# Optimization experiments

Measured on AMD Instinct MI355X. Metric: run time of the kernel, lower is better.

Reference implementation:

```python
import jax, jax.numpy as jnp
import numpy as np

N = 20000   # nodes
E = 320000  # edges (before self loops)
H = 4       # heads
HID = 64    # hidden per head
EMB = 32    # embedding dim
IN = 4      # input features
SLOPE = 0.2   # GATv2 leaky_relu negative slope
BN_EPS = 1e-5


def _gatv2(x, Wl, bl, Wr, br, att, bias, src, dst, heads, out_ch, concat, n_nodes):
    # PyG GATv2Conv (share_weights=False, add_self_loops handled by caller)
    xl = (x @ Wl.T + bl).reshape(n_nodes, heads, out_ch)  # source transform (x_j)
    xr = (x @ Wr.T + br).reshape(n_nodes, heads, out_ch)  # target transform (x_i)
    e = jax.nn.leaky_relu(xl[src] + xr[dst], SLOPE)       # [E, H, C]
    score = jnp.einsum('ehc,hc->eh', e, att)              # [E, H]
    smax = jax.ops.segment_max(score, dst, num_segments=n_nodes)
    expw = jnp.exp(score - smax[dst])
    denom = jax.ops.segment_sum(expw, dst, num_segments=n_nodes)
    alpha = expw / (denom[dst] + 1e-16)                   # segment softmax over dst
    out = jax.ops.segment_sum(xl[src] * alpha[:, :, None], dst, num_segments=n_nodes)
    out = out.reshape(n_nodes, heads * out_ch) if concat else out.mean(axis=1)
    return out + bias


def _bn(x, gamma, beta, mean, var):
    # BatchNorm1d, eval mode (running stats)
    return gamma * (x - mean) * jax.lax.rsqrt(var + BN_EPS) + beta


def setup_inputs() -> dict:
    key = jax.random.key(0)
    ks = iter(jax.random.split(key, 40))
    d = {}
    d['x'] = jax.random.normal(next(ks), (N, IN), dtype=jnp.float32)
    d['edge_index'] = jax.random.randint(next(ks), (2, E), 0, N, dtype=jnp.int32)

    def lin(k, o, i):
        return (jax.random.normal(k, (o, i), dtype=jnp.float32) * (1.0 / np.sqrt(i)))

    d['Wl1'] = lin(next(ks), H * HID, IN); d['bl1'] = jnp.zeros((H * HID,), jnp.float32)
    d['Wr1'] = lin(next(ks), H * HID, IN); d['br1'] = jnp.zeros((H * HID,), jnp.float32)
    d['att1'] = jax.random.normal(next(ks), (H, HID), dtype=jnp.float32) * 0.1
    d['bias1'] = jnp.zeros((H * HID,), jnp.float32)
    d['bn1_g'] = jnp.ones((H * HID,), jnp.float32)
    d['bn1_b'] = jnp.zeros((H * HID,), jnp.float32)
    d['bn1_m'] = jax.random.normal(next(ks), (H * HID,), dtype=jnp.float32) * 0.1
    d['bn1_v'] = jax.random.uniform(next(ks), (H * HID,), dtype=jnp.float32) + 0.5

    d['Wl2'] = lin(next(ks), H * HID, H * HID); d['bl2'] = jnp.zeros((H * HID,), jnp.float32)
    d['Wr2'] = lin(next(ks), H * HID, H * HID); d['br2'] = jnp.zeros((H * HID,), jnp.float32)
    d['att2'] = jax.random.normal(next(ks), (H, HID), dtype=jnp.float32) * 0.1
    d['bias2'] = jnp.zeros((H * HID,), jnp.float32)
    d['bn2_g'] = jnp.ones((H * HID,), jnp.float32)
    d['bn2_b'] = jnp.zeros((H * HID,), jnp.float32)
    d['bn2_m'] = jax.random.normal(next(ks), (H * HID,), dtype=jnp.float32) * 0.1
    d['bn2_v'] = jax.random.uniform(next(ks), (H * HID,), dtype=jnp.float32) + 0.5

    # layer 3: 256 -> 32, 1 head, mean (concat=False)
    d['Wl3'] = lin(next(ks), EMB, H * HID); d['bl3'] = jnp.zeros((EMB,), jnp.float32)
    d['Wr3'] = lin(next(ks), EMB, H * HID); d['br3'] = jnp.zeros((EMB,), jnp.float32)
    d['att3'] = jax.random.normal(next(ks), (1, EMB), dtype=jnp.float32) * 0.1
    d['bias3'] = jnp.zeros((EMB,), jnp.float32)
    return d


def reference(x, edge_index,
              Wl1, bl1, Wr1, br1, att1, bias1, bn1_g, bn1_b, bn1_m, bn1_v,
              Wl2, bl2, Wr2, br2, att2, bias2, bn2_g, bn2_b, bn2_m, bn2_v,
              Wl3, bl3, Wr3, br3, att3, bias3):
    # add self loops (PyG default add_self_loops=True)
    loops = jnp.arange(N, dtype=edge_index.dtype)
    src = jnp.concatenate([edge_index[0], loops])
    dst = jnp.concatenate([edge_index[1], loops])

    h = _gatv2(x, Wl1, bl1, Wr1, br1, att1, bias1, src, dst, H, HID, True, N)
    h = jax.nn.elu(_bn(h, bn1_g, bn1_b, bn1_m, bn1_v))  # dropout: eval mode -> identity
    h = _gatv2(h, Wl2, bl2, Wr2, br2, att2, bias2, src, dst, H, HID, True, N)
    h = jax.nn.elu(_bn(h, bn2_g, bn2_b, bn2_m, bn2_v))
    z = _gatv2(h, Wl3, bl3, Wr3, br3, att3, bias3, src, dst, 1, EMB, False, N)
    return z
```

## Files before the change

### kernel.cpp

```cpp
#include <hip/hip_runtime.h>
#include <math.h>

#define NN 20000
#define EE 320000
#define ETOT (EE + NN)
#define NSCAN ((NN + 1023) / 1024)

typedef unsigned short ushort_t;
typedef unsigned int uint_t;
typedef __attribute__((ext_vector_type(8))) short bf16x8;
typedef __attribute__((ext_vector_type(4))) float f32x4;

__device__ __forceinline__ ushort_t f2bf(float f) {
  union { float f; uint_t u; } v; v.f = f;
  uint_t r = v.u + 0x7FFF + ((v.u >> 16) & 1);
  return (ushort_t)(r >> 16);
}
__device__ __forceinline__ float bf2f(uint_t hi16) {
  union { uint_t u; float f; } v; v.u = hi16 << 16;
  return v.f;
}
__device__ __forceinline__ uint_t pack2(float a, float b) {
  return (uint_t)f2bf(a) | ((uint_t)f2bf(b) << 16);
}
__device__ __forceinline__ void unpack8(uint4 u, float* x) {
  x[0] = bf2f(u.x & 0xFFFF); x[1] = bf2f(u.x >> 16);
  x[2] = bf2f(u.y & 0xFFFF); x[3] = bf2f(u.y >> 16);
  x[4] = bf2f(u.z & 0xFFFF); x[5] = bf2f(u.z >> 16);
  x[6] = bf2f(u.w & 0xFFFF); x[7] = bf2f(u.w >> 16);
}

__global__ void deg_kernel(const int* __restrict__ ei, int* __restrict__ deg) {
  int e = blockIdx.x * 256 + threadIdx.x;
  if (e >= ETOT) return;
  int dst = (e < EE) ? ei[EE + e] : (e - EE);
  atomicAdd(&deg[dst], 1);
}

__global__ __launch_bounds__(1024) void scan1_kernel(const int* __restrict__ deg,
                                                     int* __restrict__ rowptr,
                                                     int* __restrict__ partials) {
  __shared__ int wsum[16];
  const int tid = threadIdx.x;
  const int lane = tid & 63, wid = tid >> 6;
  int i = blockIdx.x * 1024 + tid;
  int v = (i < NN) ? deg[i] : 0;
  int x = v;
  #pragma unroll
  for (int off = 1; off < 64; off <<= 1) {
    int y = __shfl_up(x, off, 64);
    if (lane >= off) x += y;
  }
  if (lane == 63) wsum[wid] = x;
  __syncthreads();
  if (tid < 64) {
    int w = (tid < 16) ? wsum[tid] : 0;
    #pragma unroll
    for (int off = 1; off < 16; off <<= 1) {
      int y = __shfl_up(w, off, 64);
      if (lane >= off) w += y;
    }
    if (tid < 16) wsum[tid] = w;
  }
  __syncthreads();
  int incl = x + (wid > 0 ? wsum[wid - 1] : 0);
  if (i < NN) rowptr[i] = incl - v;
  if (tid == 1023) partials[blockIdx.x] = incl;
}

__global__ void scan2_kernel(int* __restrict__ partials, int* __restrict__ rowptr) {
  int lane = threadIdx.x;
  int v = (lane < NSCAN) ? partials[lane] : 0;
  int x = v;
  #pragma unroll
  for (int off = 1; off < 64; off <<= 1) {
    int y = __shfl_up(x, off, 64);
    if (lane >= off) x += y;
  }
  if (lane < NSCAN) partials[lane] = x - v;
  if (lane == 63) rowptr[NN] = x;
}

__global__ __launch_bounds__(1024) void scan3_kernel(int* __restrict__ rowptr,
                                                     const int* __restrict__ partials,
                                                     int* __restrict__ cursor) {
  int i = blockIdx.x * 1024 + threadIdx.x;
  if (i < NN) {
    int r = rowptr[i] + partials[blockIdx.x];
    rowptr[i] = r;
    cursor[i] = r;
  }
}

__global__ void fill_kernel(const int* __restrict__ ei, int* __restrict__ cursor,
                            int* __restrict__ csr_src) {
  int e = blockIdx.x * 256 + threadIdx.x;
  if (e >= ETOT) return;
  int src, dst;
  if (e < EE) { src = ei[e]; dst = ei[EE + e]; } else { src = dst = e - EE; }
  int slot = atomicAdd(&cursor[dst], 1);
  csr_src[slot] = src;
}

__global__ void lin1_w2bf(const float* __restrict__ x,
                          const float* __restrict__ Wl, const float* __restrict__ bl,
                          const float* __restrict__ Wr, const float* __restrict__ br,
                          ushort_t* __restrict__ xlr,
                          const float* __restrict__ W0, const float* __restrict__ W1,
                          const float* __restrict__ W2, const float* __restrict__ W3,
                          ushort_t* __restrict__ Wb) {
  if (blockIdx.x >= NN) {
    int i = (blockIdx.x - NN) * 256 + threadIdx.x;
    if (i < 65536) Wb[i] = f2bf(W0[i]);
    else if (i < 131072) Wb[i] = f2bf(W1[i - 65536]);
    else if (i < 139264) Wb[i] = f2bf(W2[i - 131072]);
    else if (i < 147456) Wb[i] = f2bf(W3[i - 139264]);
    return;
  }
  int n = blockIdx.x, o = threadIdx.x;
  float4 xv = *reinterpret_cast<const float4*>(x + (size_t)n * 4);
  float4 wl = *reinterpret_cast<const float4*>(Wl + (size_t)o * 4);
  float4 wr = *reinterpret_cast<const float4*>(Wr + (size_t)o * 4);
  xlr[(size_t)n * 512 + o]       = f2bf(wl.x * xv.x + wl.y * xv.y + wl.z * xv.z + wl.w * xv.w + bl[o]);
  xlr[(size_t)n * 512 + 256 + o] = f2bf(wr.x * xv.x + wr.y * xv.y + wr.z * xv.z + wr.w * xv.w + br[o]);
}

template<int N, int NL, int WMW, int WNW>
__global__ __launch_bounds__(WMW * WNW * 64) void gemm_mfma(
    const ushort_t* __restrict__ X, const ushort_t* __restrict__ Wb,
    const float* __restrict__ bl, const float* __restrict__ br,
    ushort_t* __restrict__ Y, int M) {
  const int wave = threadIdx.x >> 6;
  const int lane = threadIdx.x & 63;
  const int wm = wave / WNW, wn = wave % WNW;
  const int r16 = lane & 15;
  const int koff = (lane >> 4) * 8;
  const int m0 = blockIdx.x * (WMW * 64) + wm * 64;
  const int nb = blockIdx.y * (WNW * 64) + wn * 64;

  const ushort_t* xp = X + (size_t)(m0 + r16) * 256 + koff;
  const ushort_t* wp = Wb + (size_t)(nb + r16) * 256 + koff;

  f32x4 acc[4][4] = {};
  bf16x8 A[4], B[4], An[4], Bn[4];
  #pragma unroll
  for (int i = 0; i < 4; ++i) {
    A[i] = *reinterpret_cast<const bf16x8*>(xp + i * 16 * 256);
    B[i] = *reinterpret_cast<const bf16x8*>(wp + i * 16 * 256);
  }
  #pragma unroll
  for (int t = 0; t < 8; ++t) {
    if (t < 7) {
      const int k0 = (t + 1) * 32;
      #pragma unroll
      for (int i = 0; i < 4; ++i) {
        An[i] = *reinterpret_cast<const bf16x8*>(xp + i * 16 * 256 + k0);
        Bn[i] = *reinterpret_cast<const bf16x8*>(wp + i * 16 * 256 + k0);
      }
    }
    #pragma unroll
    for (int j = 0; j < 4; ++j)
      #pragma unroll
      for (int i = 0; i < 4; ++i)
        acc[j][i] = __builtin_amdgcn_mfma_f32_16x16x32_bf16(B[j], A[i], acc[j][i], 0, 0, 0);
    #pragma unroll
    for (int i = 0; i < 4; ++i) { A[i] = An[i]; B[i] = Bn[i]; }
  }

  const int nlocal = (lane >> 4) * 2;
  #pragma unroll
  for (int j = 0; j < 4; ++j) {
    const int ncol0 = nb + j * 16 + (lane >> 4) * 4;
    const float4 bv = *reinterpret_cast<const float4*>(
        (ncol0 < NL) ? (bl + ncol0) : (br + (ncol0 - NL)));
    #pragma unroll
    for (int i = 0; i < 4; ++i) {
      int m = m0 + i * 16 + r16;
      if (m < M) {
        uint2 o;
        o.x = pack2(acc[j][i][0] + bv.x, acc[j][i][1] + bv.y);
        o.y = pack2(acc[j][i][2] + bv.z, acc[j][i][3] + bv.w);
        *reinterpret_cast<uint2*>(Y + (size_t)m * N + ncol0) = o;
      }
    }
  }
}

template<bool BN_ELU>
__global__ __launch_bounds__(256) void fused_agg4(
    const ushort_t* __restrict__ xlr,
    const int* __restrict__ rowptr, const int* __restrict__ csr_src,
    const float* __restrict__ att, const float* __restrict__ bias,
    const float* __restrict__ bn_g, const float* __restrict__ bn_b,
    const float* __restrict__ bn_m, const float* __restrict__ bn_v,
    ushort_t* __restrict__ out) {
  int n = blockIdx.x * 4 + (threadIdx.x >> 6);
  if (n >= NN) return;
  int lane = threadIdx.x & 63;
  int half = lane >> 5;
  int l32 = lane & 31;

  float xr[8], at[8];
  {
    uint4 xru = reinterpret_cast<const uint4*>(xlr + (size_t)n * 512 + 256)[l32];
    unpack8(xru, xr);
    float4 a0 = reinterpret_cast<const float4*>(att)[l32 * 2];
    float4 a1 = reinterpret_cast<const float4*>(att)[l32 * 2 + 1];
    at[0] = a0.x; at[1] = a0.y; at[2] = a0.z; at[3] = a0.w;
    at[4] = a1.x; at[5] = a1.y; at[6] = a1.z; at[7] = a1.w;
  }
  int beg = rowptr[n], end = rowptr[n + 1];

  float m = -3.4e38f, d = 0.f;
  float acc[8] = {0.f, 0.f, 0.f, 0.f, 0.f, 0.f, 0.f, 0.f};

  for (int s = beg + half; s < end; s += 2) {
    int src = csr_src[s];
    uint4 xu = reinterpret_cast<const uint4*>(xlr + (size_t)src * 512)[l32];
    float x[8];
    unpack8(xu, x);
    float sc = 0.f;
    #pragma unroll
    for (int c = 0; c < 8; ++c) {
      float e = x[c] + xr[c];
      e = fmaxf(e, 0.2f * e);
      sc = fmaf(at[c], e, sc);
    }
    #pragma unroll
    for (int off = 4; off; off >>= 1) sc += __shfl_xor(sc, off, 64);
    if (__any(sc > m + 8.f)) {
      float mn = fmaxf(m, sc);
      float scl = __expf(m - mn);
      float w = __expf(sc - mn);
      #pragma unroll
      for (int c = 0; c < 8; ++c) acc[c] = fmaf(w, x[c], acc[c] * scl);
      d = d * scl + w;
      m = mn;
    } else {
      float w = __expf(sc - m);
      #pragma unroll
      for (int c = 0; c < 8; ++c) acc[c] = fmaf(w, x[c], acc[c]);
      d += w;
    }
  }

  {
    float mo = __shfl_xor(m, 32, 64);
    float doo = __shfl_xor(d, 32, 64);
    float ao[8];
    #pragma unroll
    for (int c = 0; c < 8; ++c) ao[c] = __shfl_xor(acc[c], 32, 64);
    if (doo > 0.f) {
      if (d > 0.f) {
        float mn = fmaxf(m, mo);
        float se = __expf(m - mn), so = __expf(mo - mn);
        #pragma unroll
        for (int c = 0; c < 8; ++c) acc[c] = acc[c] * se + ao[c] * so;
        d = d * se + doo * so;
      } else {
        #pragma unroll
        for (int c = 0; c < 8; ++c) acc[c] = ao[c];
        d = doo;
      }
    }
  }

  if (half == 0) {
    float inv = 1.f / (d + 1e-16f);
    float4 b0 = reinterpret_cast<const float4*>(bias)[l32 * 2];
    float4 b1 = reinterpret_cast<const float4*>(bias)[l32 * 2 + 1];
    float v[8];
    v[0] = acc[0] * inv + b0.x; v[1] = acc[1] * inv + b0.y;
    v[2] = acc[2] * inv + b0.z; v[3] = acc[3] * inv + b0.w;
    v[4] = acc[4] * inv + b1.x; v[5] = acc[5] * inv + b1.y;
    v[6] = acc[6] * inv + b1.z; v[7] = acc[7] * inv + b1.w;
    if (BN_ELU) {
      float4 g0 = reinterpret_cast<const float4*>(bn_g)[l32 * 2];
      float4 g1 = reinterpret_cast<const float4*>(bn_g)[l32 * 2 + 1];
      float4 bb0 = reinterpret_cast<const float4*>(bn_b)[l32 * 2];
      float4 bb1 = reinterpret_cast<const float4*>(bn_b)[l32 * 2 + 1];
      float4 mu0 = reinterpret_cast<const float4*>(bn_m)[l32 * 2];
      float4 mu1 = reinterpret_cast<const float4*>(bn_m)[l32 * 2 + 1];
      float4 va0 = reinterpret_cast<const float4*>(bn_v)[l32 * 2];
      float4 va1 = reinterpret_cast<const float4*>(bn_v)[l32 * 2 + 1];
      float g[8] = {g0.x, g0.y, g0.z, g0.w, g1.x, g1.y, g1.z, g1.w};
      float bb[8] = {bb0.x, bb0.y, bb0.z, bb0.w, bb1.x, bb1.y, bb1.z, bb1.w};
      float mu[8] = {mu0.x, mu0.y, mu0.z, mu0.w, mu1.x, mu1.y, mu1.z, mu1.w};
      float va[8] = {va0.x, va0.y, va0.z, va0.w, va1.x, va1.y, va1.z, va1.w};
      #pragma unroll
      for (int c = 0; c < 8; ++c) {
        float sc = g[c] * rsqrtf(va[c] + 1e-5f);
        float t = sc * (v[c] - mu[c]) + bb[c];
        v[c] = (t > 0.f) ? t : expm1f(t);
      }
    }
    uint4 o;
    o.x = pack2(v[0], v[1]);
    o.y = pack2(v[2], v[3]);
    o.z = pack2(v[4], v[5]);
    o.w = pack2(v[6], v[7]);
    reinterpret_cast<uint4*>(out + (size_t)n * 256)[l32] = o;
  }
}

__global__ __launch_bounds__(256) void fused_agg3(
    const ushort_t* __restrict__ xlr,
    const int* __restrict__ rowptr, const int* __restrict__ csr_src,
    const float* __restrict__ att, const float* __restrict__ bias,
    float* __restrict__ out) {
  int n = blockIdx.x * 4 + (threadIdx.x >> 6);
  if (n >= NN) return;
  int lane = threadIdx.x & 63;
  int grp = lane >> 4;
  int cl = lane & 15;
  uint_t xru = reinterpret_cast<const uint_t*>(xlr + (size_t)n * 64 + 32)[cl];
  float xr0 = bf2f(xru & 0xFFFF), xr1 = bf2f(xru >> 16);
  float2 atv = reinterpret_cast<const float2*>(att)[cl];
  int beg = rowptr[n], end = rowptr[n + 1];
  float m = -3.4e38f, d = 0.f, a0 = 0.f, a1 = 0.f;
  for (int s = beg + grp; s < end; s += 4) {
    int src = csr_src[s];
    uint_t xu = reinterpret_cast<const uint_t*>(xlr + (size_t)src * 64)[cl];
    float x0 = bf2f(xu & 0xFFFF), x1 = bf2f(xu >> 16);
    float e0 = x0 + xr0; e0 = fmaxf(e0, 0.2f * e0);
    float e1 = x1 + xr1; e1 = fmaxf(e1, 0.2f * e1);
    float sc = fmaf(atv.x, e0, atv.y * e1);
    #pragma unroll
    for (int off = 8; off; off >>= 1) sc += __shfl_xor(sc, off, 64);
    if (__any(sc > m + 8.f)) {
      float mn = fmaxf(m, sc);
      float scale = __expf(m - mn);
      float w = __expf(sc - mn);
      a0 = fmaf(w, x0, a0 * scale);
      a1 = fmaf(w, x1, a1 * scale);
      d = d * scale + w;
      m = mn;
    } else {
      float w = __expf(sc - m);
      a0 = fmaf(w, x0, a0);
      a1 = fmaf(w, x1, a1);
      d += w;
    }
  }
  #pragma unroll
  for (int off = 16; off <= 32; off <<= 1) {
    float mo = __shfl_xor(m, off, 64);
    float doo = __shfl_xor(d, off, 64);
    float c0 = __shfl_xor(a0, off, 64);
    float c1 = __shfl_xor(a1, off, 64);
    if (doo > 0.f) {
      if (d > 0.f) {
        float mn = fmaxf(m, mo);
        float se = __expf(m - mn), so = __expf(mo - mn);
        a0 = a0 * se + c0 * so;
        a1 = a1 * se + c1 * so;
        d = d * se + doo * so;
        m = mn;
      } else {
        a0 = c0; a1 = c1; d = doo; m = mo;
      }
    }
  }
  if (grp == 0) {
    float inv = 1.f / (d + 1e-16f);
    float2 bsv = reinterpret_cast<const float2*>(bias)[cl];
    reinterpret_cast<float2*>(out + (size_t)n * 32)[cl] =
        make_float2(a0 * inv + bsv.x, a1 * inv + bsv.y);
  }
}

extern "C" void kernel_launch(void* const* d_in, const int* in_sizes, int n_in,
                              void* d_out, int out_size, void* d_ws, size_t ws_size,
                              hipStream_t stream) {
  (void)in_sizes; (void)n_in; (void)out_size; (void)ws_size;
  const float* x  = (const float*)d_in[0];
  const int*   ei = (const int*)d_in[1];
  const float *Wl1 = (const float*)d_in[2],  *bl1 = (const float*)d_in[3],
              *Wr1 = (const float*)d_in[4],  *br1 = (const float*)d_in[5],
              *att1 = (const float*)d_in[6], *bias1 = (const float*)d_in[7],
              *g1 = (const float*)d_in[8],   *be1 = (const float*)d_in[9],
              *m1 = (const float*)d_in[10],  *v1 = (const float*)d_in[11];
  const float *Wl2 = (const float*)d_in[12], *bl2 = (const float*)d_in[13],
              *Wr2 = (const float*)d_in[14], *br2 = (const float*)d_in[15],
              *att2 = (const float*)d_in[16], *bias2 = (const float*)d_in[17],
              *g2 = (const float*)d_in[18],  *be2 = (const float*)d_in[19],
              *m2 = (const float*)d_in[20],  *v2 = (const float*)d_in[21];
  const float *Wl3 = (const float*)d_in[22], *bl3 = (const float*)d_in[23],
              *Wr3 = (const float*)d_in[24], *br3 = (const float*)d_in[25],
              *att3 = (const float*)d_in[26], *bias3 = (const float*)d_in[27];
  float* out = (float*)d_out;

  char* p = (char*)d_ws;
  auto alloc = [&](size_t bytes) { char* r = p; p += (bytes + 255) & ~(size_t)255; return r; };
  int*      deg      = (int*)alloc((size_t)NN * 4);
  int*      rowptr   = (int*)alloc((size_t)(NN + 1) * 4);
  int*      cursor   = (int*)alloc((size_t)NN * 4);
  int*      partials = (int*)alloc((size_t)NSCAN * 4);
  int*      csr_src  = (int*)alloc((size_t)ETOT * 4);
  ushort_t* xlr      = (ushort_t*)alloc((size_t)NN * 512 * 2);
  ushort_t* hbuf     = (ushort_t*)alloc((size_t)NN * 256 * 2);
  ushort_t* Wb       = (ushort_t*)alloc((size_t)147456 * 2);
  (void)alloc(262144);

  hipMemsetAsync(deg, 0, (size_t)NN * 4, stream);
  deg_kernel<<<(ETOT + 255) / 256, 256, 0, stream>>>(ei, deg);
  scan1_kernel<<<NSCAN, 1024, 0, stream>>>(deg, rowptr, partials);
  scan2_kernel<<<1, 64, 0, stream>>>(partials, rowptr);
  scan3_kernel<<<NSCAN, 1024, 0, stream>>>(rowptr, partials, cursor);
  fill_kernel<<<(ETOT + 255) / 256, 256, 0, stream>>>(ei, cursor, csr_src);

  int nb = (NN + 3) / 4;

  lin1_w2bf<<<NN + 576, 256, 0, stream>>>(x, Wl1, bl1, Wr1, br1, xlr,
                                          Wl2, Wr2, Wl3, Wr3, Wb);
  fused_agg4<true><<<nb, 256, 0, stream>>>(xlr, rowptr, csr_src, att1, bias1,
                                           g1, be1, m1, v1, hbuf);

  {
    dim3 g((NN + 63) / 64, 2);
    gemm_mfma<512, 256, 1, 4><<<g, 256, 0, stream>>>(hbuf, Wb, bl2, br2, xlr, NN);
  }
  fused_agg4<true><<<nb, 256, 0, stream>>>(xlr, rowptr, csr_src, att2, bias2,
                                           g2, be2, m2, v2, hbuf);

  {
    dim3 g((NN + 255) / 256, 1);
    gemm_mfma<64, 32, 4, 1><<<g, 256, 0, stream>>>(hbuf, Wb + 131072, bl3, br3, xlr, NN);
  }
  fused_agg3<<<nb, 256, 0, stream>>>(xlr, rowptr, csr_src, att3, bias3, out);
}
```

Baseline: 206.4 us.

## Rewrite leaky-ReLU score as abs plus precomputed linear term in base-2 softmax

Uses leaky_relu(e) = 0.6*e + 0.4*|e| to split the attention score into a per-source linear term (precomputed per node and head into a small buffer, scaled by log2(e)) and an abs term computed per edge, with exp replaced by exp2 via constant folding. The target-side linear term is dropped because it is constant per destination and cancels in the softmax. The two-kernel scan merge folds scan2 into scan3 by having each block reduce the preceding partials itself. This adds a pp_kernel launch and an extra per-edge load of the precomputed scalar, and rounding behaviour changes slightly.

```diff
diff --git a/kernel.cpp b/kernel.cpp
--- a/kernel.cpp
+++ b/kernel.cpp
@@ -5,6 +5,9 @@
 #define EE 320000
 #define ETOT (EE + NN)
 #define NSCAN ((NN + 1023) / 1024)
+
+#define C_SEP 0.86561702f
+#define C_ABS 0.57707802f
 
 typedef unsigned short ushort_t;
 typedef unsigned int uint_t;
@@ -68,28 +71,26 @@
   if (tid == 1023) partials[blockIdx.x] = incl;
 }
 
-__global__ void scan2_kernel(int* __restrict__ partials, int* __restrict__ rowptr) {
-  int lane = threadIdx.x;
-  int v = (lane < NSCAN) ? partials[lane] : 0;
-  int x = v;
-  #pragma unroll
-  for (int off = 1; off < 64; off <<= 1) {
-    int y = __shfl_up(x, off, 64);
-    if (lane >= off) x += y;
-  }
-  if (lane < NSCAN) partials[lane] = x - v;
-  if (lane == 63) rowptr[NN] = x;
-}
-
 __global__ __launch_bounds__(1024) void scan3_kernel(int* __restrict__ rowptr,
                                                      const int* __restrict__ partials,
                                                      int* __restrict__ cursor) {
-  int i = blockIdx.x * 1024 + threadIdx.x;
+  __shared__ int off_s;
+  int tid = threadIdx.x;
+  if (tid < 64) {
+    int v = (tid < NSCAN && tid < (int)blockIdx.x) ? partials[tid] : 0;
+    #pragma unroll
+    for (int o = 32; o; o >>= 1) v += __shfl_xor(v, o, 64);
+    if (tid == 0) off_s = v;
+  }
+  __syncthreads();
+  int off = off_s;
+  int i = blockIdx.x * 1024 + tid;
   if (i < NN) {
-    int r = rowptr[i] + partials[blockIdx.x];
+    int r = rowptr[i] + off;
     rowptr[i] = r;
     cursor[i] = r;
   }
+  if (blockIdx.x == NSCAN - 1 && tid == 0) rowptr[NN] = off + partials[NSCAN - 1];
 }
 
 __global__ void fill_kernel(const int* __restrict__ ei, int* __restrict__ cursor,
@@ -105,7 +106,8 @@
 __global__ void lin1_w2bf(const float* __restrict__ x,
                           const float* __restrict__ Wl, const float* __restrict__ bl,
                           const float* __restrict__ Wr, const float* __restrict__ br,
-                          ushort_t* __restrict__ xlr,
+                          const float* __restrict__ att, ushort_t* __restrict__ xlr,
+                          float* __restrict__ pl,
                           const float* __restrict__ W0, const float* __restrict__ W1,
                           const float* __restrict__ W2, const float* __restrict__ W3,
                           ushort_t* __restrict__ Wb) {
@@ -121,8 +123,33 @@
   float4 xv = *reinterpret_cast<const float4*>(x + (size_t)n * 4);
   float4 wl = *reinterpret_cast<const float4*>(Wl + (size_t)o * 4);
   float4 wr = *reinterpret_cast<const float4*>(Wr + (size_t)o * 4);
-  xlr[(size_t)n * 512 + o]       = f2bf(wl.x * xv.x + wl.y * xv.y + wl.z * xv.z + wl.w * xv.w + bl[o]);
-  xlr[(size_t)n * 512 + 256 + o] = f2bf(wr.x * xv.x + wr.y * xv.y + wr.z * xv.z + wr.w * xv.w + br[o]);
+  ushort_t vlb = f2bf(wl.x * xv.x + wl.y * xv.y + wl.z * xv.z + wl.w * xv.w + bl[o]);
+  ushort_t vrb = f2bf(wr.x * xv.x + wr.y * xv.y + wr.z * xv.z + wr.w * xv.w + br[o]);
+  xlr[(size_t)n * 512 + o]       = vlb;
+  xlr[(size_t)n * 512 + 256 + o] = vrb;
+  float sl = att[o] * bf2f(vlb);
+  #pragma unroll
+  for (int off = 32; off; off >>= 1) sl += __shfl_xor(sl, off, 64);
+  if ((o & 63) == 0) pl[n * 4 + (o >> 6)] = sl * C_SEP;
+}
+
+__global__ __launch_bounds__(256) void pp_kernel(const ushort_t* __restrict__ xlr,
+                                                 const float* __restrict__ att,
+                                                 float* __restrict__ pl) {
+  int lane = threadIdx.x & 63;
+  int half = lane >> 5, l32 = lane & 31;
+  int n = blockIdx.x * 8 + (threadIdx.x >> 6) * 2 + half;
+  if (n >= NN) return;
+  uint4 u = reinterpret_cast<const uint4*>(xlr + (size_t)n * 512)[l32];
+  float xv[8];
+  unpack8(u, xv);
+  float4 a0 = reinterpret_cast<const float4*>(att)[l32 * 2];
+  float4 a1 = reinterpret_cast<const float4*>(att)[l32 * 2 + 1];
+  float s = a0.x * xv[0] + a0.y * xv[1] + a0.z * xv[2] + a0.w * xv[3]
+          + a1.x * xv[4] + a1.y * xv[5] + a1.z * xv[6] + a1.w * xv[7];
+  #pragma unroll
+  for (int off = 4; off; off >>= 1) s += __shfl_xor(s, off, 64);
+  if ((l32 & 7) == 0) pl[n * 4 + (l32 >> 3)] = s * C_SEP;
 }
 
 template<int N, int NL, int WMW, int WNW>
@@ -167,7 +194,6 @@
     for (int i = 0; i < 4; ++i) { A[i] = An[i]; B[i] = Bn[i]; }
   }
 
-  const int nlocal = (lane >> 4) * 2;
   #pragma unroll
   for (int j = 0; j < 4; ++j) {
     const int ncol0 = nb + j * 16 + (lane >> 4) * 4;
@@ -188,7 +214,7 @@
 
 template<bool BN_ELU>
 __global__ __launch_bounds__(256) void fused_agg4(
-    const ushort_t* __restrict__ xlr,
+    const ushort_t* __restrict__ xlr, const float* __restrict__ pl,
     const int* __restrict__ rowptr, const int* __restrict__ csr_src,
     const float* __restrict__ att, const float* __restrict__ bias,
     const float* __restrict__ bn_g, const float* __restrict__ bn_b,
@@ -199,6 +225,7 @@
   int lane = threadIdx.x & 63;
   int half = lane >> 5;
   int l32 = lane & 31;
+  int head = l32 >> 3;
 
   float xr[8], at[8];
   {
@@ -206,8 +233,8 @@
     unpack8(xru, xr);
     float4 a0 = reinterpret_cast<const float4*>(att)[l32 * 2];
     float4 a1 = reinterpret_cast<const float4*>(att)[l32 * 2 + 1];
-    at[0] = a0.x; at[1] = a0.y; at[2] = a0.z; at[3] = a0.w;
-    at[4] = a1.x; at[5] = a1.y; at[6] = a1.z; at[7] = a1.w;
+    at[0] = a0.x * C_ABS; at[1] = a0.y * C_ABS; at[2] = a0.z * C_ABS; at[3] = a0.w * C_ABS;
+    at[4] = a1.x * C_ABS; at[5] = a1.y * C_ABS; at[6] = a1.z * C_ABS; at[7] = a1.w * C_ABS;
   }
   int beg = rowptr[n], end = rowptr[n + 1];
 
@@ -217,27 +244,28 @@
   for (int s = beg + half; s < end; s += 2) {
     int src = csr_src[s];
     uint4 xu = reinterpret_cast<const uint4*>(xlr + (size_t)src * 512)[l32];
+    float plv = pl[src * 4 + head];
     float x[8];
     unpack8(xu, x);
     float sc = 0.f;
     #pragma unroll
     for (int c = 0; c < 8; ++c) {
       float e = x[c] + xr[c];
-      e = fmaxf(e, 0.2f * e);
-      sc = fmaf(at[c], e, sc);
+      sc = fmaf(at[c], fabsf(e), sc);
     }
     #pragma unroll
     for (int off = 4; off; off >>= 1) sc += __shfl_xor(sc, off, 64);
-    if (__any(sc > m + 8.f)) {
+    sc += plv;
+    if (__any(sc > m + 11.6f)) {
       float mn = fmaxf(m, sc);
-      float scl = __expf(m - mn);
-      float w = __expf(sc - mn);
+      float scl = exp2f(m - mn);
+      float w = exp2f(sc - mn);
       #pragma unroll
       for (int c = 0; c < 8; ++c) acc[c] = fmaf(w, x[c], acc[c] * scl);
       d = d * scl + w;
       m = mn;
     } else {
-      float w = __expf(sc - m);
+      float w = exp2f(sc - m);
       #pragma unroll
       for (int c = 0; c < 8; ++c) acc[c] = fmaf(w, x[c], acc[c]);
       d += w;
@@ -253,7 +281,7 @@
     if (doo > 0.f) {
       if (d > 0.f) {
         float mn = fmaxf(m, mo);
-        float se = __expf(m - mn), so = __expf(mo - mn);
+        float se = exp2f(m - mn), so = exp2f(mo - mn);
         #pragma unroll
         for (int c = 0; c < 8; ++c) acc[c] = acc[c] * se + ao[c] * so;
         d = d * se + doo * so;
@@ -400,27 +428,28 @@
   ushort_t* xlr      = (ushort_t*)alloc((size_t)NN * 512 * 2);
   ushort_t* hbuf     = (ushort_t*)alloc((size_t)NN * 256 * 2);
   ushort_t* Wb       = (ushort_t*)alloc((size_t)147456 * 2);
+  float*    pl       = (float*)alloc((size_t)NN * 4 * 4);
   (void)alloc(262144);
 
   hipMemsetAsync(deg, 0, (size_t)NN * 4, stream);
   deg_kernel<<<(ETOT + 255) / 256, 256, 0, stream>>>(ei, deg);
   scan1_kernel<<<NSCAN, 1024, 0, stream>>>(deg, rowptr, partials);
-  scan2_kernel<<<1, 64, 0, stream>>>(partials, rowptr);
   scan3_kernel<<<NSCAN, 1024, 0, stream>>>(rowptr, partials, cursor);
   fill_kernel<<<(ETOT + 255) / 256, 256, 0, stream>>>(ei, cursor, csr_src);
 
   int nb = (NN + 3) / 4;
 
-  lin1_w2bf<<<NN + 576, 256, 0, stream>>>(x, Wl1, bl1, Wr1, br1, xlr,
+  lin1_w2bf<<<NN + 576, 256, 0, stream>>>(x, Wl1, bl1, Wr1, br1, att1, xlr, pl,
                                           Wl2, Wr2, Wl3, Wr3, Wb);
-  fused_agg4<true><<<nb, 256, 0, stream>>>(xlr, rowptr, csr_src, att1, bias1,
+  fused_agg4<true><<<nb, 256, 0, stream>>>(xlr, pl, rowptr, csr_src, att1, bias1,
                                            g1, be1, m1, v1, hbuf);
 
   {
     dim3 g((NN + 63) / 64, 2);
     gemm_mfma<512, 256, 1, 4><<<g, 256, 0, stream>>>(hbuf, Wb, bl2, br2, xlr, NN);
   }
-  fused_agg4<true><<<nb, 256, 0, stream>>>(xlr, rowptr, csr_src, att2, bias2,
+  pp_kernel<<<(NN + 7) / 8, 256, 0, stream>>>(xlr, att2, pl);
+  fused_agg4<true><<<nb, 256, 0, stream>>>(xlr, pl, rowptr, csr_src, att2, bias2,
                                            g2, be2, m2, v2, hbuf);
 
   {
```

Result: no change. 210.1 us (+1.8%).
